# Optimization experiments

Hardware: AMD Instinct MI355X
Metric: run time of the kernel (lower is better)

## Reference

```python
import jax, jax.numpy as jnp
import numpy as np

B, LQ, LKV = 8, 512, 512
D, H, DH, FF = 1024, 16, 64, 4096
CH, CHID = 16, 32  # AttentionBiasMLP channels
EPS_LOG = 1e-6
EPS_LN = 1e-6


def _ln(x, g, b):
    mu = jnp.mean(x, axis=-1, keepdims=True)
    var = jnp.var(x, axis=-1, keepdims=True)
    return (x - mu) * jax.lax.rsqrt(var + EPS_LN) * g + b


def setup_inputs() -> dict:
    key = jax.random.key(0)
    ks = jax.random.split(key, 24)
    s = 0.02
    inp = {
        "q": jax.random.normal(ks[0], (B, LQ, D), jnp.float32),
        "kv": jax.random.normal(ks[1], (B, LKV, D), jnp.float32),
        "attn_map": jax.random.uniform(ks[2], (B, CH, LQ + 1, LKV + 1), jnp.float32),
        # attention projections (torch Linear: y = x @ W.T + b)
        "Wq": jax.random.normal(ks[3], (D, D)) * s, "bq": jnp.zeros((D,)),
        "Wk": jax.random.normal(ks[4], (D, D)) * s, "bk": jnp.zeros((D,)),
        "Wv": jax.random.normal(ks[5], (D, D)) * s, "bv": jnp.zeros((D,)),
        "Wm": jax.random.normal(ks[6], (D, D)) * s, "bm": jnp.zeros((D,)),
        # AttentionBiasMLP 1x1 convs: weight [out_ch, in_ch]
        "Wc1": jax.random.normal(ks[7], (CHID, CH)) * s, "bc1": jnp.zeros((CHID,)),
        "Wc2": jax.random.normal(ks[8], (CH, CHID)) * s, "bc2": jnp.zeros((CH,)),
        # FFN: Linear(D,FF) -> ReLU -> Linear(FF,D)
        "Wf1": jax.random.normal(ks[9], (FF, D)) * s, "bf1": jnp.zeros((FF,)),
        "Wf2": jax.random.normal(ks[10], (D, FF)) * s, "bf2": jnp.zeros((D,)),
        # LayerNorms
        "g1": jnp.ones((D,)), "b1": jnp.zeros((D,)),
        "g2": jnp.ones((D,)), "b2": jnp.zeros((D,)),
    }
    return inp


def _forward(q, kv, attn_map, Wq, bq, Wk, bk, Wv, bv, Wm, bm,
             Wc1, bc1, Wc2, bc2, Wf1, bf1, Wf2, bf2, g1, b1, g2, b2):
    # attention bias: log of cropped attn_map through 1x1-conv MLP with exact GELU
    log_map = jnp.log(attn_map[:, :, 1:, 1:] + EPS_LOG)               # [B,CH,LQ,LKV]
    h = jnp.einsum('bcqk,oc->boqk', log_map, Wc1) + bc1[None, :, None, None]
    h = jax.nn.gelu(h, approximate=False)
    attn_bias = jnp.einsum('bcqk,oc->boqk', h, Wc2) + bc2[None, :, None, None]

    # MHAtt: project, split heads
    qh = (q @ Wq.T + bq).reshape(B, LQ, H, DH).transpose(0, 2, 1, 3)   # [B,H,LQ,DH]
    kh = (kv @ Wk.T + bk).reshape(B, LKV, H, DH).transpose(0, 2, 1, 3)
    vh = (kv @ Wv.T + bv).reshape(B, LKV, H, DH).transpose(0, 2, 1, 3)

    scores = jnp.einsum('bhqd,bhkd->bhqk', qh, kh) / np.sqrt(DH).astype(np.float32)
    scores = scores + attn_bias
    att = jax.nn.softmax(scores, axis=-1)
    ctx = jnp.einsum('bhqk,bhkd->bhqd', att, vh)                       # [B,H,LQ,DH]
    ctx = ctx.transpose(0, 2, 1, 3).reshape(B, LQ, D)
    atted = ctx @ Wm.T + bm

    x = _ln(q + atted, g1, b1)
    ffn = jax.nn.relu(x @ Wf1.T + bf1) @ Wf2.T + bf2
    x = _ln(x + ffn, g2, b2)
    return x


def reference(q, kv, attn_map, Wq, bq, Wk, bk, Wv, bv, Wm, bm,
              Wc1, bc1, Wc2, bc2, Wf1, bf1, Wf2, bf2, g1, b1, g2, b2):
    return _forward(q, kv, attn_map, Wq, bq, Wk, bk, Wv, bv, Wm, bm,
                    Wc1, bc1, Wc2, bc2, Wf1, bf1, Wf2, bf2, g1, b1, g2, b2)
```

## Files before the change

### kernel.cpp

```cpp
#include <hip/hip_runtime.h>
#include <hip/hip_bf16.h>

typedef __bf16 bf16_t;
typedef __bf16 bf16x4_t __attribute__((ext_vector_type(4)));
typedef __bf16 bf16x8_t __attribute__((ext_vector_type(8)));
typedef float  f32x4_t  __attribute__((ext_vector_type(4)));

#define B_   8
#define LQ_  512
#define LKV_ 512
#define D_   1024
#define H_   16
#define DH_  64
#define FF_  4096

__device__ __forceinline__ f32x4_t mfma16(bf16x8_t a, bf16x8_t b, f32x4_t c) {
    return __builtin_amdgcn_mfma_f32_16x16x32_bf16(a, b, c, 0, 0, 0);
}

__device__ __forceinline__ void gload_lds16(const bf16_t* g, bf16_t* l) {
    __builtin_amdgcn_global_load_lds(
        (const __attribute__((address_space(1))) void*)g,
        (__attribute__((address_space(3))) void*)l, 16, 0, 0);
}

__device__ __forceinline__ int xcd_swz(int pid, int nwg) {
    return (pid & 7) * (nwg >> 3) + (pid >> 3);
}

__device__ __forceinline__ float gelu_fast(float h) {
    const float e = exp2f(h * -2.45546696f);
    return h * __builtin_amdgcn_rcpf(1.f + e);
}

__global__ __launch_bounds__(256)
void cvt_bf16_kernel(const float* __restrict__ in, bf16_t* __restrict__ out, int n4) {
    const int i = blockIdx.x * 256 + threadIdx.x;
    if (i >= n4) return;
    const float4 v = ((const float4*)in)[i];
    bf16x4_t o;
    o[0] = (bf16_t)v.x; o[1] = (bf16_t)v.y; o[2] = (bf16_t)v.z; o[3] = (bf16_t)v.w;
    ((bf16x4_t*)out)[i] = o;
}

__global__ __launch_bounds__(256)
void pack3_kernel(const float* __restrict__ a, const float* __restrict__ b,
                  const float* __restrict__ c, float* __restrict__ o) {
    const int i = blockIdx.x * 256 + threadIdx.x;
    o[i] = a[i]; o[1024 + i] = b[i]; o[2048 + i] = c[i];
}

__global__ __launch_bounds__(256)
void bias_mlp_mfma(const float* __restrict__ amap,
                   const float* __restrict__ Wc1, const float* __restrict__ bc1,
                   const float* __restrict__ Wc2, const float* __restrict__ bc2,
                   bf16_t* __restrict__ biasb) {
    __shared__ __align__(16) char lds[4][8192];
    const int t = threadIdx.x, lane = t & 63, w = t >> 6;
    const int l15 = lane & 15, lg = lane >> 4;
    char* Xs = lds[w];
    char* Hs = lds[w] + 3072;

    bf16x8_t b1f[2], b2f;
    f32x4_t bc1v[2];
#pragma unroll
    for (int ot = 0; ot < 2; ot++) {
        bf16x8_t v;
#pragma unroll
        for (int i = 0; i < 8; i++) {
            const int kk = (lg * 8 + i) & 15;
            const float wv = Wc1[(ot * 16 + l15) * 16 + kk] * 0.69314718055994531f;
            v[i] = (lg < 2) ? (bf16_t)wv : (bf16_t)0.f;
        }
        b1f[ot] = v;
        const float bb = bc1[ot * 16 + l15];
        bc1v[ot] = f32x4_t{bb, bb, bb, bb};
    }
    {
        bf16x8_t v;
#pragma unroll
        for (int i = 0; i < 8; i++) v[i] = (bf16_t)Wc2[l15 * 32 + lg * 8 + i];
        b2f = v;
    }
    const float bc2s = bc2[l15];
    const f32x4_t cinit2 = f32x4_t{bc2s, bc2s, bc2s, bc2s};

    const int posb = (blockIdx.x * 4 + w) * 64;
    const int b  = posb >> 18;
    const int q  = (posb >> 9) & 511;
    const int k0 = posb & 511;

    const float* src = amap + (size_t)(b * 16) * 263169 + (size_t)(q + 1) * 513 + (k0 + 1 + lane);
    bf16_t xr[16];
#pragma unroll
    for (int c = 0; c < 16; c++) {
        const float v = src[(size_t)c * 263169];
        xr[c] = (bf16_t)__log2f(v + 1e-6f);
    }
    *(bf16x8_t*)(Xs + lane * 48)      = *(bf16x8_t*)&xr[0];
    *(bf16x8_t*)(Xs + lane * 48 + 16) = *(bf16x8_t*)&xr[8];

    const int lgm16 = (lg & 1) * 16;
    f32x4_t h1[4][2];
#pragma unroll
    for (int p = 0; p < 4; p++) {
        const bf16x8_t a1 = *(const bf16x8_t*)(Xs + (p * 16 + l15) * 48 + lgm16);
#pragma unroll
        for (int ot = 0; ot < 2; ot++)
            h1[p][ot] = mfma16(a1, b1f[ot], bc1v[ot]);
    }

#pragma unroll
    for (int p = 0; p < 4; p++)
#pragma unroll
        for (int ot = 0; ot < 2; ot++)
#pragma unroll
            for (int r = 0; r < 4; r++) {
                const float g = gelu_fast(h1[p][ot][r]);
                *(bf16_t*)(Hs + (p * 16 + lg * 4 + r) * 80 + (ot * 16 + l15) * 2) = (bf16_t)g;
            }

    const size_t obase = ((size_t)(b * 16 + l15) * 512 + q) * 512 + k0;
#pragma unroll
    for (int p = 0; p < 4; p++) {
        const bf16x8_t a2 = *(const bf16x8_t*)(Hs + (p * 16 + l15) * 80 + lg * 16);
        const f32x4_t o2 = mfma16(a2, b2f, cinit2);
        bf16x4_t ov;
#pragma unroll
        for (int r = 0; r < 4; r++) ov[r] = (bf16_t)o2[r];
        *(bf16x4_t*)&biasb[obase + p * 16 + lg * 4] = ov;
    }
}

template <int EPI, bool SPLIT>
__global__ __launch_bounds__(256)
void gemm_bt(const bf16_t* __restrict__ A, const bf16_t* __restrict__ A2,
             const bf16_t* __restrict__ Bw,
             const float* __restrict__ bias, float* __restrict__ Cf,
             bf16_t* __restrict__ Cb, int M, int N, int Klen, int lda) {
    __shared__ __align__(16) bf16_t As[128 * 32];
    __shared__ __align__(16) bf16_t Bs[128 * 32];
    const int t = threadIdx.x, lane = t & 63, w = t >> 6;
    const int wr = w >> 1, wc = w & 1;
    const int ntn = N >> 7;
    const int nwg = (M >> 7) * ntn;
    const int wg  = xcd_swz((int)blockIdx.x, nwg);
    const int gsz = 8 * ntn;
    const int gid = wg / gsz;
    const int rem = wg - gid * gsz;
    const int tm  = gid * 8 + (rem & 7);
    const int tn  = rem >> 3;
    const int l15 = lane & 15, lg = lane >> 4;
    const int ks = SPLIT ? blockIdx.y : 0;
    const int koff = SPLIT ? ks * Klen : 0;
    if (EPI == 3 && tn >= 8) A = A2;

    f32x4_t acc[4][4];
#pragma unroll
    for (int i = 0; i < 4; i++)
#pragma unroll
        for (int j = 0; j < 4; j++) acc[i][j] = f32x4_t{0.f, 0.f, 0.f, 0.f};

    const int nk = Klen >> 5;
    for (int kt = 0; kt < nk; ++kt) {
#pragma unroll
        for (int i = 0; i < 2; i++) {
            const int c = i * 256 + w * 64 + lane;
            const int c0 = i * 256 + w * 64;
            const int row = c >> 2, kg = c & 3;
            gload_lds16(A + (size_t)(tm * 128 + row) * lda + koff + kt * 32 + kg * 8, &As[c0 * 8]);
        }
#pragma unroll
        for (int i = 0; i < 2; i++) {
            const int c = i * 256 + w * 64 + lane;
            const int c0 = i * 256 + w * 64;
            const int row = c >> 2, kg = c & 3;
            gload_lds16(Bw + (size_t)(tn * 128 + row) * lda + koff + kt * 32 + kg * 8, &Bs[c0 * 8]);
        }
        __syncthreads();

        bf16x8_t af[4], bfv[4];
#pragma unroll
        for (int mt = 0; mt < 4; mt++)
            af[mt] = *(const bf16x8_t*)&As[(wr * 64 + mt * 16 + l15) * 32 + lg * 8];
#pragma unroll
        for (int nt = 0; nt < 4; nt++)
            bfv[nt] = *(const bf16x8_t*)&Bs[(wc * 64 + nt * 16 + l15) * 32 + lg * 8];
#pragma unroll
        for (int mt = 0; mt < 4; mt++)
#pragma unroll
            for (int nt = 0; nt < 4; nt++)
                acc[mt][nt] = mfma16(af[mt], bfv[nt], acc[mt][nt]);
        __syncthreads();
    }

#pragma unroll
    for (int nt = 0; nt < 4; nt++) {
        const int col = tn * 128 + wc * 64 + nt * 16 + l15;
        float bv = bias[col];
        if (SPLIT && ks != 0) bv = 0.f;
#pragma unroll
        for (int mt = 0; mt < 4; mt++) {
#pragma unroll
            for (int r = 0; r < 4; r++) {
                const int row = tm * 128 + wr * 64 + mt * 16 + lg * 4 + r;
                float v = acc[mt][nt][r] + bv;
                if (EPI == 2) v = fmaxf(v, 0.f);
                if (EPI == 3 && tn < 8) v *= 0.125f;
                if (EPI == 0) Cf[(size_t)ks * M * N + (size_t)row * N + col] = v;
                else if (EPI == 3)
                    Cb[(size_t)(col >> 10) * 4194304 + (size_t)row * 1024 + (col & 1023)] = (bf16_t)v;
                else Cb[(size_t)row * N + col] = (bf16_t)v;
            }
        }
    }
}

__global__ __launch_bounds__(256)
void attn_kernel(const bf16_t* __restrict__ Qp, const bf16_t* __restrict__ Kp,
                 const bf16_t* __restrict__ Vp, const bf16_t* __restrict__ biasb,
                 bf16_t* __restrict__ ctx) {
    __shared__ __align__(16) bf16_t Qs[64 * 64];
    __shared__ __align__(16) bf16_t Ks[64 * 64];
    __shared__ __align__(16) bf16_t Vts[64 * 64];
    __shared__ __align__(16) bf16_t Ps[64 * 64];
    __shared__ __align__(16) bf16_t Bbs[64 * 64];

    const int bid = xcd_swz((int)blockIdx.x, 1024);
    const int qt = bid & 7, h = (bid >> 3) & 15, b = bid >> 7;
    const int t = threadIdx.x, lane = t & 63, w = t >> 6;
    const int l15 = lane & 15, lg = lane >> 4;

#pragma unroll
    for (int i = 0; i < 2; i++) {
        const int c = t + i * 256;
        const int row = c >> 3, cg = c & 7;
        const uint4 v = *(const uint4*)&Qp[(((size_t)(b * LQ_ + qt * 64 + row)) * H_ + h) * DH_ + cg * 8];
        *(uint4*)((char*)Qs + row * 128 + ((cg ^ (row & 7)) << 4)) = v;
    }

    f32x4_t oacc[4];
#pragma unroll
    for (int i = 0; i < 4; i++) oacc[i] = f32x4_t{0.f, 0.f, 0.f, 0.f};
    float mrow[4] = {-1e30f, -1e30f, -1e30f, -1e30f};
    float lrow[4] = {0.f, 0.f, 0.f, 0.f};

    const bf16_t* bias_tile = biasb + ((size_t)(b * H_ + h) * LQ_ + qt * 64) * LKV_;

    for (int kt = 0; kt < 8; ++kt) {
        __syncthreads();
#pragma unroll
        for (int i = 0; i < 2; i++) {
            const int c = t + i * 256;
            const int row = c >> 3, cg = c & 7;
            const uint4 v = *(const uint4*)&Kp[(((size_t)(b * LKV_ + kt * 64 + row)) * H_ + h) * DH_ + cg * 8];
            *(uint4*)((char*)Ks + row * 128 + ((cg ^ (row & 7)) << 4)) = v;
        }
#pragma unroll
        for (int i = 0; i < 2; i++) {
            const int c = t + i * 256;
            const int row = c >> 3, cg = c & 7;
            const uint4 bv4 = *(const uint4*)&bias_tile[(size_t)row * LKV_ + kt * 64 + cg * 8];
            *(uint4*)&Bbs[row * 64 + cg * 8] = bv4;
        }
#pragma unroll
        for (int i = 0; i < 2; i++) {
            const int c = t + i * 256;
            const int k = c >> 3, dg = c & 7;
            const bf16x8_t vv = *(const bf16x8_t*)&Vp[(((size_t)(b * LKV_ + kt * 64 + k)) * H_ + h) * DH_ + dg * 8];
#pragma unroll
            for (int j = 0; j < 8; j++) {
                const int d = dg * 8 + j;
                *(bf16_t*)((char*)Vts + d * 128 + ((((k * 2) >> 4) ^ (d & 7)) << 4) + ((k * 2) & 15)) = vv[j];
            }
        }
        __syncthreads();

        f32x4_t sacc[4];
#pragma unroll
        for (int i = 0; i < 4; i++) sacc[i] = f32x4_t{0.f, 0.f, 0.f, 0.f};
        bf16x8_t aq[2];
        {
            const int rowq = w * 16 + l15;
#pragma unroll
            for (int kc = 0; kc < 2; kc++)
                aq[kc] = *(const bf16x8_t*)((const char*)Qs + rowq * 128 + (((kc * 4 + lg) ^ (rowq & 7)) << 4));
        }
#pragma unroll
        for (int nt = 0; nt < 4; nt++) {
            const int rowk = nt * 16 + l15;
#pragma unroll
            for (int kc = 0; kc < 2; kc++) {
                const bf16x8_t bk = *(const bf16x8_t*)((const char*)Ks + rowk * 128 + (((kc * 4 + lg) ^ (rowk & 7)) << 4));
                sacc[nt] = mfma16(aq[kc], bk, sacc[nt]);
            }
        }

        float esc[4];
#pragma unroll
        for (int r = 0; r < 4; r++) {
            const int qr = w * 16 + lg * 4 + r;
            float mx = -1e30f;
#pragma unroll
            for (int nt = 0; nt < 4; nt++) {
                const float bvv = (float)Bbs[qr * 64 + nt * 16 + l15];
                const float v = sacc[nt][r] + bvv;
                sacc[nt][r] = v;
                mx = fmaxf(mx, v);
            }
#pragma unroll
            for (int msk = 8; msk >= 1; msk >>= 1) mx = fmaxf(mx, __shfl_xor(mx, msk));
            const float mnew = fmaxf(mrow[r], mx);
            esc[r] = __expf(mrow[r] - mnew);
            mrow[r] = mnew;
            float rs = 0.f;
#pragma unroll
            for (int nt = 0; nt < 4; nt++) {
                const float p = __expf(sacc[nt][r] - mnew);
                sacc[nt][r] = p;
                rs += p;
            }
#pragma unroll
            for (int msk = 8; msk >= 1; msk >>= 1) rs += __shfl_xor(rs, msk);
            lrow[r] = lrow[r] * esc[r] + rs;
        }

#pragma unroll
        for (int r = 0; r < 4; r++) {
            const int prow = w * 16 + lg * 4 + r;
#pragma unroll
            for (int nt = 0; nt < 4; nt++) {
                const int pc2 = (nt * 16 + l15) * 2;
                *(bf16_t*)((char*)Ps + prow * 128 + (((pc2 >> 4) ^ (prow & 7)) << 4) + (pc2 & 15)) =
                    (bf16_t)sacc[nt][r];
            }
        }
        asm volatile("s_waitcnt lgkmcnt(0)" ::: "memory");
        __builtin_amdgcn_sched_barrier(0);

#pragma unroll
        for (int dt = 0; dt < 4; dt++)
#pragma unroll
            for (int r = 0; r < 4; r++) oacc[dt][r] *= esc[r];

        bf16x8_t pa[2];
        {
            const int rowp = w * 16 + l15;
#pragma unroll
            for (int kc = 0; kc < 2; kc++)
                pa[kc] = *(const bf16x8_t*)((const char*)Ps + rowp * 128 + (((kc * 4 + lg) ^ (rowp & 7)) << 4));
        }
#pragma unroll
        for (int dt = 0; dt < 4; dt++) {
            const int rowv = dt * 16 + l15;
#pragma unroll
            for (int kc = 0; kc < 2; kc++) {
                const bf16x8_t bv = *(const bf16x8_t*)((const char*)Vts + rowv * 128 + (((kc * 4 + lg) ^ (rowv & 7)) << 4));
                oacc[dt] = mfma16(pa[kc], bv, oacc[dt]);
            }
        }
    }

    float inv[4];
#pragma unroll
    for (int r = 0; r < 4; r++) inv[r] = __builtin_amdgcn_rcpf(lrow[r]);
#pragma unroll
    for (int dt = 0; dt < 4; dt++) {
#pragma unroll
        for (int r = 0; r < 4; r++) {
            const float v = oacc[dt][r] * inv[r];
            const int q = qt * 64 + w * 16 + lg * 4 + r;
            const int d = dt * 16 + l15;
            ctx[(((size_t)(b * LQ_ + q)) * H_ + h) * DH_ + d] = (bf16_t)v;
        }
    }
}

__global__ __launch_bounds__(256)
void add_ln3_kernel(const float* __restrict__ X, const float* __restrict__ Y0,
                    const float* __restrict__ Y1,
                    const float* __restrict__ g, const float* __restrict__ be,
                    float* __restrict__ of, bf16_t* __restrict__ ob) {
    const int row = blockIdx.x, t = threadIdx.x;
    const float4 xv = ((const float4*)(X + (size_t)row * 1024))[t];
    const float4 y0 = ((const float4*)(Y0 + (size_t)row * 1024))[t];
    const float4 y1 = ((const float4*)(Y1 + (size_t)row * 1024))[t];
    float v[4] = {xv.x + y0.x + y1.x, xv.y + y0.y + y1.y,
                  xv.z + y0.z + y1.z, xv.w + y0.w + y1.w};
    float s = v[0] + v[1] + v[2] + v[3];
    float s2 = v[0] * v[0] + v[1] * v[1] + v[2] * v[2] + v[3] * v[3];
#pragma unroll
    for (int m = 32; m >= 1; m >>= 1) { s += __shfl_xor(s, m); s2 += __shfl_xor(s2, m); }
    __shared__ float red[8];
    const int w = t >> 6, lane = t & 63;
    if (lane == 0) { red[w] = s; red[4 + w] = s2; }
    __syncthreads();
    s = red[0] + red[1] + red[2] + red[3];
    s2 = red[4] + red[5] + red[6] + red[7];
    const float mu = s * (1.f / 1024.f);
    const float var = s2 * (1.f / 1024.f) - mu * mu;
    const float rstd = rsqrtf(var + 1e-6f);
    const float4 gv = ((const float4*)g)[t];
    const float4 bv = ((const float4*)be)[t];
    float o[4];
    o[0] = (v[0] - mu) * rstd * gv.x + bv.x;
    o[1] = (v[1] - mu) * rstd * gv.y + bv.y;
    o[2] = (v[2] - mu) * rstd * gv.z + bv.z;
    o[3] = (v[3] - mu) * rstd * gv.w + bv.w;
    ((float4*)(of + (size_t)row * 1024))[t] = make_float4(o[0], o[1], o[2], o[3]);
    if (ob) {
        bf16x4_t qo;
        qo[0] = (bf16_t)o[0]; qo[1] = (bf16_t)o[1]; qo[2] = (bf16_t)o[2]; qo[3] = (bf16_t)o[3];
        ((bf16x4_t*)(ob + (size_t)row * 1024))[t] = qo;
    }
}

extern "C" void kernel_launch(void* const* d_in, const int* in_sizes, int n_in,
                              void* d_out, int out_size, void* d_ws, size_t ws_size,
                              hipStream_t stream) {
    (void)in_sizes; (void)n_in; (void)out_size; (void)ws_size;
    const float* q    = (const float*)d_in[0];
    const float* kv   = (const float*)d_in[1];
    const float* amap = (const float*)d_in[2];
    const float* Wq = (const float*)d_in[3];  const float* bQ = (const float*)d_in[4];
    const float* Wk = (const float*)d_in[5];  const float* bK = (const float*)d_in[6];
    const float* Wv = (const float*)d_in[7];  const float* bV = (const float*)d_in[8];
    const float* Wm = (const float*)d_in[9];  const float* bM = (const float*)d_in[10];
    const float* Wc1 = (const float*)d_in[11]; const float* bc1 = (const float*)d_in[12];
    const float* Wc2 = (const float*)d_in[13]; const float* bc2 = (const float*)d_in[14];
    const float* Wf1 = (const float*)d_in[15]; const float* bf1 = (const float*)d_in[16];
    const float* Wf2 = (const float*)d_in[17]; const float* bf2 = (const float*)d_in[18];
    const float* g1 = (const float*)d_in[19]; const float* b1 = (const float*)d_in[20];
    const float* g2 = (const float*)d_in[21]; const float* b2 = (const float*)d_in[22];

    char* w = (char*)d_ws;
    bf16_t* biasb = (bf16_t*)(w);
    float*  p0    = (float*)(w);
    float*  p1    = (float*)(w + 16777216);
    bf16_t* hb    = (bf16_t*)(w);
    float*  f0    = (float*)(w + 33554432);
    float*  f1    = (float*)(w + 50331648);
    bf16_t* qb   = (bf16_t*)(w + 67108864);
    bf16_t* kvb  = (bf16_t*)(w + 75497472);
    bf16_t* Qp   = (bf16_t*)(w + 83886080);
    bf16_t* Kp   = (bf16_t*)(w + 92274688);
    bf16_t* Vp   = (bf16_t*)(w + 100663296);
    bf16_t* Wqkvb = (bf16_t*)(w + 109051904);
    bf16_t* Wmb  = (bf16_t*)(w + 115343360);
    bf16_t* Wf1b = (bf16_t*)(w + 117440512);
    bf16_t* Wf2b = (bf16_t*)(w + 125829120);
    float*  bqkv = (float*)(w + 134217728);
    bf16_t* ctx = qb;
    float*  xf  = (float*)Qp;
    bf16_t* xb  = Vp;

    dim3 blk(256);
    cvt_bf16_kernel<<<4096, blk, 0, stream>>>(q,   qb,   1048576);
    cvt_bf16_kernel<<<4096, blk, 0, stream>>>(kv,  kvb,  1048576);
    cvt_bf16_kernel<<<1024, blk, 0, stream>>>(Wq,  Wqkvb,           262144);
    cvt_bf16_kernel<<<1024, blk, 0, stream>>>(Wk,  Wqkvb + 1048576, 262144);
    cvt_bf16_kernel<<<1024, blk, 0, stream>>>(Wv,  Wqkvb + 2097152, 262144);
    cvt_bf16_kernel<<<1024, blk, 0, stream>>>(Wm,  Wmb,  262144);
    cvt_bf16_kernel<<<4096, blk, 0, stream>>>(Wf1, Wf1b, 1048576);
    cvt_bf16_kernel<<<4096, blk, 0, stream>>>(Wf2, Wf2b, 1048576);
    pack3_kernel<<<4, blk, 0, stream>>>(bQ, bK, bV, bqkv);

    bias_mlp_mfma<<<8192, blk, 0, stream>>>(amap, Wc1, bc1, Wc2, bc2, biasb);

    gemm_bt<3, false><<<768, blk, 0, stream>>>(qb, kvb, Wqkvb, bqkv, nullptr, Qp,
                                               4096, 3072, 1024, 1024);

    attn_kernel<<<1024, blk, 0, stream>>>(Qp, Kp, Vp, biasb, ctx);

    gemm_bt<0, true><<<dim3(256, 2), blk, 0, stream>>>(ctx, nullptr, Wmb, bM, p0, nullptr,
                                                       4096, 1024, 512, 1024);
    add_ln3_kernel<<<4096, blk, 0, stream>>>(q, p0, p1, g1, b1, xf, xb);

    gemm_bt<2, false><<<1024, blk, 0, stream>>>(xb, nullptr, Wf1b, bf1, nullptr, hb,
                                                4096, 4096, 1024, 1024);
    gemm_bt<0, true><<<dim3(256, 2), blk, 0, stream>>>(hb, nullptr, Wf2b, bf2, f0, nullptr,
                                                       4096, 1024, 2048, 4096);
    add_ln3_kernel<<<4096, blk, 0, stream>>>(xf, f0, f1, g2, b2, (float*)d_out, nullptr);
}
```

Before: 364.1 us.

## Double-buffer GEMM LDS tiles and fuse fp32-to-bf16 conversions into one launch

The GEMM kernel now uses two LDS buffers per operand, issuing global-to-LDS loads for the next K tile before computing MFMAs on the current one. This leaves one barrier per iteration instead of two. The eight separate conversion launches are merged into a single kernel that picks its source and destination by index range. The cost is doubled LDS per block (32 KB), which may reduce occupancy, and a branchy dispatch inside the conversion kernel.

```diff
diff --git a/kernel.cpp b/kernel.cpp
--- a/kernel.cpp
+++ b/kernel.cpp
@@ -34,13 +34,26 @@
 }
 
 __global__ __launch_bounds__(256)
-void cvt_bf16_kernel(const float* __restrict__ in, bf16_t* __restrict__ out, int n4) {
+void cvt_all_kernel(const float* __restrict__ q,  const float* __restrict__ kv,
+                    const float* __restrict__ Wq, const float* __restrict__ Wk,
+                    const float* __restrict__ Wv, const float* __restrict__ Wm,
+                    const float* __restrict__ Wf1,const float* __restrict__ Wf2,
+                    bf16_t* __restrict__ dq, bf16_t* __restrict__ dW,
+                    bf16_t* __restrict__ dF) {
     const int i = blockIdx.x * 256 + threadIdx.x;
-    if (i >= n4) return;
-    const float4 v = ((const float4*)in)[i];
+    const float* s; bf16_t* d; int j;
+    if (i < 1048576)      { s = q;   d = dq;           j = i; }
+    else if (i < 2097152) { s = kv;  d = dq + 4194304; j = i - 1048576; }
+    else if (i < 2359296) { s = Wq;  d = dW;           j = i - 2097152; }
+    else if (i < 2621440) { s = Wk;  d = dW + 1048576; j = i - 2359296; }
+    else if (i < 2883584) { s = Wv;  d = dW + 2097152; j = i - 2621440; }
+    else if (i < 3145728) { s = Wm;  d = dW + 3145728; j = i - 2883584; }
+    else if (i < 4194304) { s = Wf1; d = dF;           j = i - 3145728; }
+    else                  { s = Wf2; d = dF + 4194304; j = i - 4194304; }
+    const float4 v = ((const float4*)s)[j];
     bf16x4_t o;
     o[0] = (bf16_t)v.x; o[1] = (bf16_t)v.y; o[2] = (bf16_t)v.z; o[3] = (bf16_t)v.w;
-    ((bf16x4_t*)out)[i] = o;
+    ((bf16x4_t*)d)[j] = o;
 }
 
 __global__ __launch_bounds__(256)
@@ -138,8 +151,8 @@
              const bf16_t* __restrict__ Bw,
              const float* __restrict__ bias, float* __restrict__ Cf,
              bf16_t* __restrict__ Cb, int M, int N, int Klen, int lda) {
-    __shared__ __align__(16) bf16_t As[128 * 32];
-    __shared__ __align__(16) bf16_t Bs[128 * 32];
+    __shared__ __align__(16) bf16_t As[2][128 * 32];
+    __shared__ __align__(16) bf16_t Bs[2][128 * 32];
     const int t = threadIdx.x, lane = t & 63, w = t >> 6;
     const int wr = w >> 1, wc = w & 1;
     const int ntn = N >> 7;
@@ -155,6 +168,17 @@
     const int koff = SPLIT ? ks * Klen : 0;
     if (EPI == 3 && tn >= 8) A = A2;
 
+    const int c0_ = t;
+    const int c1_ = t + 256;
+    const int r0 = c0_ >> 2, k0 = c0_ & 3;
+    const int r1 = c1_ >> 2, k1 = c1_ & 3;
+    const int b0 = (w * 64) * 8;
+    const int b1 = (256 + w * 64) * 8;
+    const bf16_t* Abase0 = A  + (size_t)(tm * 128 + r0) * lda + koff + k0 * 8;
+    const bf16_t* Abase1 = A  + (size_t)(tm * 128 + r1) * lda + koff + k1 * 8;
+    const bf16_t* Bbase0 = Bw + (size_t)(tn * 128 + r0) * lda + koff + k0 * 8;
+    const bf16_t* Bbase1 = Bw + (size_t)(tn * 128 + r1) * lda + koff + k1 * 8;
+
     f32x4_t acc[4][4];
 #pragma unroll
     for (int i = 0; i < 4; i++)
@@ -162,36 +186,44 @@
         for (int j = 0; j < 4; j++) acc[i][j] = f32x4_t{0.f, 0.f, 0.f, 0.f};
 
     const int nk = Klen >> 5;
+
+    gload_lds16(Abase0, &As[0][b0]);
+    gload_lds16(Abase1, &As[0][b1]);
+    gload_lds16(Bbase0, &Bs[0][b0]);
+    gload_lds16(Bbase1, &Bs[0][b1]);
+    asm volatile("s_waitcnt vmcnt(0)" ::: "memory");
+    __syncthreads();
+
+    int cur = 0;
     for (int kt = 0; kt < nk; ++kt) {
-#pragma unroll
-        for (int i = 0; i < 2; i++) {
-            const int c = i * 256 + w * 64 + lane;
-            const int c0 = i * 256 + w * 64;
-            const int row = c >> 2, kg = c & 3;
-            gload_lds16(A + (size_t)(tm * 128 + row) * lda + koff + kt * 32 + kg * 8, &As[c0 * 8]);
-        }
-#pragma unroll
-        for (int i = 0; i < 2; i++) {
-            const int c = i * 256 + w * 64 + lane;
-            const int c0 = i * 256 + w * 64;
-            const int row = c >> 2, kg = c & 3;
-            gload_lds16(Bw + (size_t)(tn * 128 + row) * lda + koff + kt * 32 + kg * 8, &Bs[c0 * 8]);
-        }
-        __syncthreads();
-
+        if (kt + 1 < nk) {
+            const int ko = (kt + 1) * 32;
+            gload_lds16(Abase0 + ko, &As[cur ^ 1][b0]);
+            gload_lds16(Abase1 + ko, &As[cur ^ 1][b1]);
+            gload_lds16(Bbase0 + ko, &Bs[cur ^ 1][b0]);
+            gload_lds16(Bbase1 + ko, &Bs[cur ^ 1][b1]);
+        }
+
+        const bf16_t* Ac = As[cur];
+        const bf16_t* Bc = Bs[cur];
         bf16x8_t af[4], bfv[4];
 #pragma unroll
         for (int mt = 0; mt < 4; mt++)
-            af[mt] = *(const bf16x8_t*)&As[(wr * 64 + mt * 16 + l15) * 32 + lg * 8];
+            af[mt] = *(const bf16x8_t*)&Ac[(wr * 64 + mt * 16 + l15) * 32 + lg * 8];
 #pragma unroll
         for (int nt = 0; nt < 4; nt++)
-            bfv[nt] = *(const bf16x8_t*)&Bs[(wc * 64 + nt * 16 + l15) * 32 + lg * 8];
+            bfv[nt] = *(const bf16x8_t*)&Bc[(wc * 64 + nt * 16 + l15) * 32 + lg * 8];
 #pragma unroll
         for (int mt = 0; mt < 4; mt++)
 #pragma unroll
             for (int nt = 0; nt < 4; nt++)
                 acc[mt][nt] = mfma16(af[mt], bfv[nt], acc[mt][nt]);
-        __syncthreads();
+
+        if (kt + 1 < nk) {
+            asm volatile("s_waitcnt vmcnt(0)" ::: "memory");
+            __syncthreads();
+            cur ^= 1;
+        }
     }
 
 #pragma unroll
@@ -453,16 +485,11 @@
     bf16_t* ctx = qb;
     float*  xf  = (float*)Qp;
     bf16_t* xb  = Vp;
+    (void)Wmb; (void)Wf2b; (void)kvb;
 
     dim3 blk(256);
-    cvt_bf16_kernel<<<4096, blk, 0, stream>>>(q,   qb,   1048576);
-    cvt_bf16_kernel<<<4096, blk, 0, stream>>>(kv,  kvb,  1048576);
-    cvt_bf16_kernel<<<1024, blk, 0, stream>>>(Wq,  Wqkvb,           262144);
-    cvt_bf16_kernel<<<1024, blk, 0, stream>>>(Wk,  Wqkvb + 1048576, 262144);
-    cvt_bf16_kernel<<<1024, blk, 0, stream>>>(Wv,  Wqkvb + 2097152, 262144);
-    cvt_bf16_kernel<<<1024, blk, 0, stream>>>(Wm,  Wmb,  262144);
-    cvt_bf16_kernel<<<4096, blk, 0, stream>>>(Wf1, Wf1b, 1048576);
-    cvt_bf16_kernel<<<4096, blk, 0, stream>>>(Wf2, Wf2b, 1048576);
+    cvt_all_kernel<<<20480, blk, 0, stream>>>(q, kv, Wq, Wk, Wv, Wm, Wf1, Wf2,
+                                              qb, Wqkvb, Wf1b);
     pack3_kernel<<<4, blk, 0, stream>>>(bQ, bK, bV, bqkv);
 
     bias_mlp_mfma<<<8192, blk, 0, stream>>>(amap, Wc1, bc1, Wc2, bc2, biasb);
```

Measured after the change: 332.8 us. 1.09x faster.
